# Performance work log

Measured on AMD Instinct MI355X. Metric: run time of the kernel, lower is better.

The kernel has to match this reference:

```python
import jax, jax.numpy as jnp
import numpy as np

B, S, DA, DV, DU, L, M = 16, 256, 1, 32, 1, 4, 12


def conv1x1(x, w, b):
    # x: [B,C,H,W], w: [O,C], b: [O]
    return jnp.einsum('bchw,oc->bohw', x, w) + b[None, :, None, None]


def setup_inputs() -> dict:
    key = jax.random.key(0)
    ks = jax.random.split(key, 12)
    sc = 0.02
    return {
        'x':    jax.random.normal(ks[0], (B, S, S, DA), dtype=jnp.float32),
        'p_w':  sc * jax.random.normal(ks[1], (DV, DA + 2), dtype=jnp.float32),
        'p_b':  sc * jax.random.normal(ks[2], (DV,), dtype=jnp.float32),
        'ws_w': sc * jax.random.normal(ks[3], (L, DV, DV), dtype=jnp.float32),
        'ws_b': sc * jax.random.normal(ks[4], (L, DV), dtype=jnp.float32),
        'w1r':  sc * jax.random.normal(ks[5], (L, DV, DV, M, M), dtype=jnp.float32),
        'w1i':  sc * jax.random.normal(ks[6], (L, DV, DV, M, M), dtype=jnp.float32),
        'w2r':  sc * jax.random.normal(ks[7], (L, DV, DV, M, M), dtype=jnp.float32),
        'w2i':  sc * jax.random.normal(ks[8], (L, DV, DV, M, M), dtype=jnp.float32),
        'q_w':  sc * jax.random.normal(ks[9], (DU, DV), dtype=jnp.float32),
        'q_b':  sc * jax.random.normal(ks[10], (DU,), dtype=jnp.float32),
    }


def fourier_layer(x, w1r, w1i, w2r, w2i):
    # x: [B,C,H,W]; FFT norm None == 'backward' (numpy/jax default)
    b, c, h, w = x.shape
    x_ft = jnp.fft.rfft2(x)                       # [B,C,H,W//2+1] complex
    W1 = w1r + 1j * w1i                           # [C,C,M,M]
    W2 = w2r + 1j * w2i
    top = jnp.einsum('bixy,ioxy->boxy', x_ft[:, :, :M, :M], W1)
    bot = jnp.einsum('bixy,ioxy->boxy', x_ft[:, :, -M:, :M], W2)
    out_ft = jnp.zeros((b, c, h, w // 2 + 1), dtype=x_ft.dtype)
    out_ft = out_ft.at[:, :, :M, :M].set(top)
    out_ft = out_ft.at[:, :, h - M:, :M].set(bot)
    return jnp.fft.irfft2(out_ft, s=(h, w))


def reference(x, p_w, p_b, ws_w, ws_b, w1r, w1i, w2r, w2i, q_w, q_b):
    b, sx, sy, _ = x.shape
    # grid as in get_grid (requires sx == sy, as the original implicitly does)
    gx = jnp.linspace(-1.0, 1.0, sx, dtype=jnp.float32)
    gy = jnp.linspace(-1.0, 1.0, sy, dtype=jnp.float32)
    gridx = jnp.broadcast_to(gx.reshape(1, 1, sx, 1), (b, sy, sx, 1))
    gridy = jnp.broadcast_to(gy.reshape(1, sy, 1, 1), (b, sy, sx, 1))
    grid = jnp.concatenate([gridy, gridx], axis=-1)     # [B,Sy,Sx,2]
    h = jnp.concatenate([x, grid], axis=-1)             # [B,S,S,DA+2]
    h = jnp.transpose(h, (0, 3, 1, 2))                  # NCHW
    h = conv1x1(h, p_w, p_b)                            # lifting
    for i in range(L):
        x1 = fourier_layer(h, w1r[i], w1i[i], w2r[i], w2i[i])
        x2 = conv1x1(h, ws_w[i], ws_b[i])
        h = x1 + x2
        if i < L - 1:
            h = jax.nn.relu(h)
    h = conv1x1(h, q_w, q_b)                            # projection -> [B,1,S,S]
    return jnp.transpose(h, (0, 2, 3, 1)).squeeze(-1)   # [B,S,S]
```

## Files before the change

### kernel.cpp

```cpp
#include <hip/hip_runtime.h>
#include <math.h>

#define NB 16
#define SS 256
#define DV 32
#define MM 12
#define MK 24
#define LL 4
#define TWO_PI_N 0.024543692606170259679f
#define HSTR 257
#define TWSOFF (DV * HSTR)

typedef float v2f __attribute__((ext_vector_type(2)));


__global__ __launch_bounds__(256) void k_prep(const float* __restrict__ ws_w,
        float* __restrict__ twT, float* __restrict__ wT, float* __restrict__ tw2)
{
    int j = threadIdx.x;
    #pragma unroll
    for (int k = 0; k < MM; ++k) {
        float ang = TWO_PI_N * (float)((k * j) & 255);
        float s, c; sincosf(ang, &s, &c);
        twT[j * (MM * 2) + 2 * k]     = c;
        twT[j * (MM * 2) + 2 * k + 1] = -s;
        tw2[(k * SS + j) * 2]     = c;
        tw2[(k * SS + j) * 2 + 1] = s;
    }
    for (int idx = threadIdx.x; idx < LL * DV * DV; idx += 256) {
        int l = idx >> 10, rem = idx & 1023, co = rem >> 5, ci = rem & 31;
        wT[(l * DV + ci) * DV + co] = ws_w[(l * DV + co) * DV + ci];
    }
}

__device__ __forceinline__ void row_dft_from_lds(float* smem,
        const float* __restrict__ twT, float* __restrict__ A,
        int b, int iy, int tid)
{
    int c   = tid & 31;
    int seg = tid >> 5;
    int j0  = seg << 5;

    v2f arai[MM];
    #pragma unroll
    for (int k = 0; k < MM; ++k) arai[k] = (v2f)(0.f);

    const float* hp = smem + c * HSTR + j0;
    #pragma unroll 2
    for (int i = 0; i < 32; ++i) {
        float v = hp[i];
        const v2f* twj = (const v2f*)(twT + (size_t)i * (MM * 2));
        #pragma unroll
        for (int k = 0; k < MM; ++k)
            arai[k] += twj[k] * v;
    }

    const float* ph = smem + TWSOFF + seg * (MM * 2);
    #pragma unroll
    for (int k = 0; k < MM; ++k) {
        float pr = ph[2 * k], pi = ph[2 * k + 1];
        float re = arai[k].x * pr - arai[k].y * pi;
        float im = arai[k].x * pi + arai[k].y * pr;
        arai[k].x = re; arai[k].y = im;
    }

    __syncthreads();
    v2f* red = (v2f*)smem;
    #pragma unroll
    for (int k = 0; k < MM; ++k) red[tid * 13 + k] = arai[k];
    __syncthreads();

    #pragma unroll
    for (int rep = 0; rep < 2; ++rep) {
        int o = tid + rep * 256;
        if (o < 384) {
            int k = o >> 5, cc = o & 31;
            v2f s = (v2f)(0.f);
            #pragma unroll
            for (int sg = 0; sg < 8; ++sg)
                s += red[(sg * 32 + cc) * 13 + k];
            size_t off = ((((size_t)(b * SS + iy)) * MM + k) * DV + cc) * 2;
            A[off]     = s.x;
            A[off + 1] = s.y;
        }
    }
}

__device__ __forceinline__ void build_segphase(float* smem, int tid)
{
    if (tid < 8 * MM) {
        int s = tid / MM, k = tid - s * MM;
        float ang = TWO_PI_N * (float)(((k * s) << 5) & 255);
        float sn, cs; sincosf(ang, &sn, &cs);
        smem[TWSOFF + 2 * tid]     = cs;
        smem[TWSOFF + 2 * tid + 1] = -sn;
    }
}

__global__ __launch_bounds__(256, 4) void k_liftdft(const float* __restrict__ x,
        const float* __restrict__ p_w, const float* __restrict__ p_b,
        float* __restrict__ h, const float* __restrict__ twT, float* __restrict__ A)
{
    __shared__ float smem[DV * HSTR + 8 * MM * 2];
    int tid = threadIdx.x;
    int b  = blockIdx.x >> 8;
    int iy = blockIdx.x & 255;
    int j  = tid;

    build_segphase(smem, tid);

    float xv = x[((size_t)(b * SS + iy)) * SS + j];
    float gy = -1.f + 2.f * (float)iy * (1.f / 255.f);
    float gx = -1.f + 2.f * (float)j  * (1.f / 255.f);

    float* hb = h + ((size_t)b * DV * SS + iy) * SS + j;
    #pragma unroll
    for (int c = 0; c < DV; ++c) {
        float v = p_w[3*c] * xv + p_w[3*c+1] * gy + p_w[3*c+2] * gx + p_b[c];
        *(hb + (size_t)c * SS * SS) = v;
        smem[c * HSTR + j] = v;
    }
    __syncthreads();
    row_dft_from_lds(smem, twT, A, b, iy, tid);
}

__global__ __launch_bounds__(256, 4) void k_ptdft(float* __restrict__ h,
        const float* __restrict__ g, const float* __restrict__ wT,
        const float* __restrict__ ws_b, const float* __restrict__ tw2,
        const float* __restrict__ twT, float* __restrict__ A, int l)
{
    __shared__ float smem[DV * HSTR + 8 * MM * 2];
    int tid = threadIdx.x;
    int b  = blockIdx.x >> 8;
    int iy = blockIdx.x & 255;
    int j  = tid;

    build_segphase(smem, tid);

    float* hb = h + ((size_t)b * DV * SS + iy) * SS + j;
    const float* wt  = wT + (size_t)l * DV * DV;
    const float* wsb = ws_b + (size_t)l * DV;

    float acc[DV];
    #pragma unroll
    for (int co = 0; co < DV; ++co) acc[co] = wsb[co];

    #pragma unroll 4
    for (int ci = 0; ci < DV; ++ci) {
        float hv = *(hb + (size_t)ci * SS * SS);
        const float* wc = wt + ci * DV;
        #pragma unroll
        for (int co = 0; co < DV; ++co) acc[co] += wc[co] * hv;
    }

    const float* gp = g + ((size_t)(b * SS + iy)) * (MM * DV * 2);
    #pragma unroll 2
    for (int ky = 0; ky < MM; ++ky) {
        float2 t2 = *(const float2*)(tw2 + ((size_t)ky * SS + j) * 2);
        const float* Gk = gp + ky * (DV * 2);
        #pragma unroll
        for (int co = 0; co < DV; ++co) {
            float gr = Gk[2 * co], gi = Gk[2 * co + 1];
            acc[co] += gr * t2.x - gi * t2.y;
        }
    }

    #pragma unroll
    for (int co = 0; co < DV; ++co) {
        float v = fmaxf(acc[co], 0.f);
        *(hb + (size_t)co * SS * SS) = v;
        smem[co * HSTR + j] = v;
    }
    __syncthreads();
    row_dft_from_lds(smem, twT, A, b, iy, tid);
}

__global__ __launch_bounds__(256, 4) void k_cm(const float* __restrict__ A,
        const float* __restrict__ w1r, const float* __restrict__ w1i,
        const float* __restrict__ w2r, const float* __restrict__ w2i,
        float* __restrict__ F, int l)
{
    __shared__ float red[4][DV][7][2];
    __shared__ float FinS[DV][6][2];
    int blk = blockIdx.x;
    int mg = blk & 3;
    int bk = blk >> 2;
    int b  = bk / MM;
    int ky = bk - b * MM;
    int tid = threadIdx.x;
    int c = tid & 31, ch = tid >> 5;
    int iy0 = ch * 32;

    const float2* Ap = (const float2*)(A) + ((size_t)(b * SS) * MM + ky) * DV + c;

    float fr[6], fi[6], pc[6], ps[6], sc[6], ssn[6];
    #pragma unroll
    for (int k = 0; k < 6; ++k) {
        int m = mg * 6 + k;
        int f = (m < MM) ? m : (232 + m);
        float s, cc;
        sincosf(TWO_PI_N * (float)f, &s, &cc);
        sc[k] = cc; ssn[k] = s;
        sincosf(TWO_PI_N * (float)((f * iy0) & 255), &s, &cc);
        pc[k] = cc; ps[k] = s;
        fr[k] = fi[k] = 0.f;
    }
    #pragma unroll 4
    for (int i = 0; i < 32; ++i) {
        float2 a = Ap[(size_t)(iy0 + i) * (MM * DV)];
        #pragma unroll
        for (int k = 0; k < 6; ++k) {
            fr[k] += a.x * pc[k] + a.y * ps[k];
            fi[k] += a.y * pc[k] - a.x * ps[k];
            float np = pc[k] * sc[k] - ps[k] * ssn[k];
            float nq = pc[k] * ssn[k] + ps[k] * sc[k];
            pc[k] = np; ps[k] = nq;
        }
    }
    #pragma unroll
    for (int k = 0; k < 6; ++k) {
        fr[k] += __shfl_xor(fr[k], 32, 64);
        fi[k] += __shfl_xor(fi[k], 32, 64);
    }
    int wv = tid >> 6;
    if ((tid & 63) < 32) {
        #pragma unroll
        for (int k = 0; k < 6; ++k) {
            red[wv][c][k][0] = fr[k];
            red[wv][c][k][1] = fi[k];
        }
    }
    __syncthreads();
    if (tid < 192) {
        int cc = tid & 31, k2 = tid >> 5;
        float sr = 0.f, si = 0.f;
        #pragma unroll
        for (int w = 0; w < 4; ++w) {
            sr += red[w][cc][k2][0];
            si += red[w][cc][k2][1];
        }
        FinS[cc][k2][0] = sr; FinS[cc][k2][1] = si;
    }
    __syncthreads();

    int c2 = tid >> 3, ch2 = tid & 7;
    if (ch2 < 6) {
        int o = c2;
        int m = mg * 6 + ch2;
        const float* Wr; const float* Wi; int xm;
        if (m < MM) { Wr = w1r; Wi = w1i; xm = m; }
        else        { Wr = w2r; Wi = w2i; xm = m - MM; }
        float scale = ((ky == 0) ? 1.0f : 2.0f) * (1.0f / 65536.0f);
        float orr = 0.f, oii = 0.f;
        #pragma unroll 4
        for (int i = 0; i < DV; ++i) {
            float gr = FinS[i][ch2][0], gi = FinS[i][ch2][1];
            size_t wi = ((size_t)(l * DV + i) * DV + o) * (MM * MM) + xm * MM + ky;
            float wr = Wr[wi], wim = Wi[wi];
            orr += gr * wr - gi * wim;
            oii += gr * wim + gi * wr;
        }
        size_t off = (((size_t)bk * MK + m) * DV + o) * 2;
        F[off] = orr * scale; F[off + 1] = oii * scale;
    }
}

__global__ __launch_bounds__(384) void k_inv1(const float* __restrict__ F,
        float* __restrict__ g)
{
    __shared__ float itw[MK * 2];
    int tid = threadIdx.x;
    int b = blockIdx.x >> 8, iy = blockIdx.x & 255;
    if (tid < MK) {
        int f = (tid < MM) ? tid : (232 + tid);
        float ang = TWO_PI_N * (float)((f * iy) & 255);
        float s, c; sincosf(ang, &s, &c);
        itw[2 * tid] = c; itw[2 * tid + 1] = s;
    }
    __syncthreads();

    int ky = tid >> 5, co = tid & 31;
    const float* Fp = F + ((size_t)(b * MM + ky) * MK) * (DV * 2) + 2 * co;
    float gr = 0.f, gi = 0.f;
    #pragma unroll
    for (int m = 0; m < MK; ++m) {
        float2 fv = *(const float2*)(Fp + (size_t)m * (DV * 2));
        float ic = itw[2 * m], is = itw[2 * m + 1];
        gr += fv.x * ic - fv.y * is;
        gi += fv.x * is + fv.y * ic;
    }
    size_t o = (((size_t)(b * SS + iy)) * MM + ky) * (DV * 2) + 2 * co;
    g[o] = gr; g[o + 1] = gi;
}

template<int FINAL>
__global__ __launch_bounds__(256, 4) void k_pt(float* __restrict__ h,
        const float* __restrict__ g, const float* __restrict__ wT,
        const float* __restrict__ ws_b, const float* __restrict__ tw2,
        const float* __restrict__ q_w, const float* __restrict__ q_b,
        float* __restrict__ out, int l)
{
    int tid = threadIdx.x;
    int lane = tid & 63;
    int w = __builtin_amdgcn_readfirstlane(tid >> 6);
    int b  = blockIdx.x >> 7;
    int iy = ((blockIdx.x & 127) << 1) + (w >> 1);
    int j0 = ((w & 1) << 7) + (lane << 1);

    float* hb = h + ((size_t)b * DV * SS + iy) * SS + j0;
    const float* wt  = wT + (size_t)l * DV * DV;
    const float* wsb = ws_b + (size_t)l * DV;

    float2 acc[DV];
    #pragma unroll
    for (int co = 0; co < DV; ++co) {
        float bv = wsb[co];
        acc[co].x = bv; acc[co].y = bv;
    }

    #pragma unroll 4
    for (int ci = 0; ci < DV; ++ci) {
        float2 hv = *(const float2*)(hb + (size_t)ci * SS * SS);
        const float* wc = wt + ci * DV;
        #pragma unroll
        for (int co = 0; co < DV; ++co) {
            float wv = wc[co];
            acc[co].x += wv * hv.x; acc[co].y += wv * hv.y;
        }
    }

    const float* gp = g + ((size_t)(b * SS + iy)) * (MM * DV * 2);
    #pragma unroll 2
    for (int ky = 0; ky < MM; ++ky) {
        float4 t4 = *(const float4*)(tw2 + ((size_t)ky * SS + j0) * 2);
        const float* Gk = gp + ky * (DV * 2);
        #pragma unroll
        for (int co = 0; co < DV; ++co) {
            float gr = Gk[2 * co], gi = Gk[2 * co + 1];
            acc[co].x += gr * t4.x - gi * t4.y;
            acc[co].y += gr * t4.z - gi * t4.w;
        }
    }

    if (FINAL) {
        float qb = q_b[0];
        float2 o2; o2.x = qb; o2.y = qb;
        #pragma unroll
        for (int co = 0; co < DV; ++co) {
            float qv = q_w[co];
            o2.x += qv * acc[co].x; o2.y += qv * acc[co].y;
        }
        *(float2*)(out + ((size_t)(b * SS + iy)) * SS + j0) = o2;
    } else {
        #pragma unroll
        for (int co = 0; co < DV; ++co) {
            float2 v;
            v.x = fmaxf(acc[co].x, 0.f); v.y = fmaxf(acc[co].y, 0.f);
            *(float2*)(hb + (size_t)co * SS * SS) = v;
        }
    }
}

extern "C" void kernel_launch(void* const* d_in, const int* in_sizes, int n_in,
                              void* d_out, int out_size, void* d_ws, size_t ws_size,
                              hipStream_t stream)
{
    const float* x    = (const float*)d_in[0];
    const float* p_w  = (const float*)d_in[1];
    const float* p_b  = (const float*)d_in[2];
    const float* ws_w = (const float*)d_in[3];
    const float* ws_b = (const float*)d_in[4];
    const float* w1r  = (const float*)d_in[5];
    const float* w1i  = (const float*)d_in[6];
    const float* w2r  = (const float*)d_in[7];
    const float* w2i  = (const float*)d_in[8];
    const float* q_w  = (const float*)d_in[9];
    const float* q_b  = (const float*)d_in[10];
    float* out = (float*)d_out;

    float* h   = (float*)d_ws;
    float* A   = h   + (size_t)NB * DV * SS * SS;
    float* F   = A   + (size_t)NB * SS * MM * DV * 2;
    float* g   = F   + (size_t)NB * MM * MK * DV * 2;
    float* twT = g   + (size_t)NB * SS * MM * DV * 2;
    float* wT  = twT + (size_t)SS * MM * 2;
    float* tw2 = wT  + (size_t)LL * DV * DV;

    dim3 blk(256);
    k_prep<<<1, blk, 0, stream>>>(ws_w, twT, wT, tw2);
    k_liftdft<<<NB * SS, blk, 0, stream>>>(x, p_w, p_b, h, twT, A);
    for (int l = 0; l < LL; ++l) {
        k_cm<<<NB * MM * 4, blk, 0, stream>>>(A, w1r, w1i, w2r, w2i, F, l);
        k_inv1<<<NB * SS, dim3(384), 0, stream>>>(F, g);
        if (l < LL - 1)
            k_ptdft<<<NB * SS, blk, 0, stream>>>(h, g, wT, ws_b, tw2, twT, A, l);
        else
            k_pt<1><<<NB * 128, blk, 0, stream>>>(h, g, wT, ws_b, tw2,
                                                  q_w, q_b, out, l);
    }
}
```

Before: 677.5 us.

## Fuse inverse column DFT into pointwise kernels via shared memory

Removes the separate k_inv1 launch and the global g buffer. Each pointwise block (k_ptdft and the final projection kernel) now recomputes its row's inverse DFT over the 24 retained modes from F directly into LDS. This drops one launch per layer and the write and read of g, in exchange for extra shared memory, an added barrier and some per-block setup latency.

```diff
diff --git a/kernel.cpp b/kernel.cpp
--- a/kernel.cpp
+++ b/kernel.cpp
@@ -9,7 +9,9 @@
 #define LL 4
 #define TWO_PI_N 0.024543692606170259679f
 #define HSTR 257
-#define TWSOFF (DV * HSTR)
+#define SEGOFF (DV * HSTR)
+#define GOFF   (SEGOFF + 8*MM*2)
+#define ITWOFF (GOFF + MM*DV*2)
 
 typedef float v2f __attribute__((ext_vector_type(2)));
 
@@ -55,7 +57,7 @@
             arai[k] += twj[k] * v;
     }
 
-    const float* ph = smem + TWSOFF + seg * (MM * 2);
+    const float* ph = smem + SEGOFF + seg * (MM * 2);
     #pragma unroll
     for (int k = 0; k < MM; ++k) {
         float pr = ph[2 * k], pi = ph[2 * k + 1];
@@ -92,8 +94,8 @@
         int s = tid / MM, k = tid - s * MM;
         float ang = TWO_PI_N * (float)(((k * s) << 5) & 255);
         float sn, cs; sincosf(ang, &sn, &cs);
-        smem[TWSOFF + 2 * tid]     = cs;
-        smem[TWSOFF + 2 * tid + 1] = -sn;
+        smem[SEGOFF + 2 * tid]     = cs;
+        smem[SEGOFF + 2 * tid + 1] = -sn;
     }
 }
 
@@ -101,7 +103,7 @@
         const float* __restrict__ p_w, const float* __restrict__ p_b,
         float* __restrict__ h, const float* __restrict__ twT, float* __restrict__ A)
 {
-    __shared__ float smem[DV * HSTR + 8 * MM * 2];
+    __shared__ float smem[SEGOFF + 8 * MM * 2];
     int tid = threadIdx.x;
     int b  = blockIdx.x >> 8;
     int iy = blockIdx.x & 255;
@@ -125,17 +127,43 @@
 }
 
 __global__ __launch_bounds__(256, 4) void k_ptdft(float* __restrict__ h,
-        const float* __restrict__ g, const float* __restrict__ wT,
+        const float* __restrict__ F, const float* __restrict__ wT,
         const float* __restrict__ ws_b, const float* __restrict__ tw2,
         const float* __restrict__ twT, float* __restrict__ A, int l)
 {
-    __shared__ float smem[DV * HSTR + 8 * MM * 2];
+    __shared__ float smem[ITWOFF + MK * 2];
     int tid = threadIdx.x;
     int b  = blockIdx.x >> 8;
     int iy = blockIdx.x & 255;
     int j  = tid;
 
     build_segphase(smem, tid);
+    if (tid < MK) {
+        int f = (tid < MM) ? tid : (232 + tid);
+        float s, c; sincosf(TWO_PI_N * (float)((f * iy) & 255), &s, &c);
+        smem[ITWOFF + 2 * tid]     = c;
+        smem[ITWOFF + 2 * tid + 1] = s;
+    }
+    __syncthreads();
+
+    #pragma unroll
+    for (int rep = 0; rep < 2; ++rep) {
+        int o = tid + rep * 256;
+        if (o < MM * DV) {
+            int ky = o >> 5, co = o & 31;
+            const float* Fp = F + ((size_t)(b * MM + ky) * MK) * (DV * 2) + 2 * co;
+            float gr = 0.f, gi = 0.f;
+            #pragma unroll
+            for (int m = 0; m < MK; ++m) {
+                float2 fv = *(const float2*)(Fp + (size_t)m * (DV * 2));
+                float ic = smem[ITWOFF + 2 * m], is = smem[ITWOFF + 2 * m + 1];
+                gr += fv.x * ic - fv.y * is;
+                gi += fv.x * is + fv.y * ic;
+            }
+            smem[GOFF + 2 * o]     = gr;
+            smem[GOFF + 2 * o + 1] = gi;
+        }
+    }
 
     float* hb = h + ((size_t)b * DV * SS + iy) * SS + j;
     const float* wt  = wT + (size_t)l * DV * DV;
@@ -153,11 +181,12 @@
         for (int co = 0; co < DV; ++co) acc[co] += wc[co] * hv;
     }
 
-    const float* gp = g + ((size_t)(b * SS + iy)) * (MM * DV * 2);
+    __syncthreads();
+
     #pragma unroll 2
     for (int ky = 0; ky < MM; ++ky) {
         float2 t2 = *(const float2*)(tw2 + ((size_t)ky * SS + j) * 2);
-        const float* Gk = gp + ky * (DV * 2);
+        const float* Gk = smem + GOFF + ky * (DV * 2);
         #pragma unroll
         for (int co = 0; co < DV; ++co) {
             float gr = Gk[2 * co], gi = Gk[2 * co + 1];
@@ -265,47 +294,47 @@
     }
 }
 
-__global__ __launch_bounds__(384) void k_inv1(const float* __restrict__ F,
-        float* __restrict__ g)
-{
-    __shared__ float itw[MK * 2];
-    int tid = threadIdx.x;
-    int b = blockIdx.x >> 8, iy = blockIdx.x & 255;
-    if (tid < MK) {
-        int f = (tid < MM) ? tid : (232 + tid);
-        float ang = TWO_PI_N * (float)((f * iy) & 255);
-        float s, c; sincosf(ang, &s, &c);
-        itw[2 * tid] = c; itw[2 * tid + 1] = s;
-    }
-    __syncthreads();
-
-    int ky = tid >> 5, co = tid & 31;
-    const float* Fp = F + ((size_t)(b * MM + ky) * MK) * (DV * 2) + 2 * co;
-    float gr = 0.f, gi = 0.f;
-    #pragma unroll
-    for (int m = 0; m < MK; ++m) {
-        float2 fv = *(const float2*)(Fp + (size_t)m * (DV * 2));
-        float ic = itw[2 * m], is = itw[2 * m + 1];
-        gr += fv.x * ic - fv.y * is;
-        gi += fv.x * is + fv.y * ic;
-    }
-    size_t o = (((size_t)(b * SS + iy)) * MM + ky) * (DV * 2) + 2 * co;
-    g[o] = gr; g[o + 1] = gi;
-}
-
-template<int FINAL>
-__global__ __launch_bounds__(256, 4) void k_pt(float* __restrict__ h,
-        const float* __restrict__ g, const float* __restrict__ wT,
+__global__ __launch_bounds__(256, 4) void k_ptfin(float* __restrict__ h,
+        const float* __restrict__ F, const float* __restrict__ wT,
         const float* __restrict__ ws_b, const float* __restrict__ tw2,
         const float* __restrict__ q_w, const float* __restrict__ q_b,
         float* __restrict__ out, int l)
 {
+    __shared__ float s2[2 * MK * 2 + 2 * MM * DV * 2];
     int tid = threadIdx.x;
     int lane = tid & 63;
     int w = __builtin_amdgcn_readfirstlane(tid >> 6);
-    int b  = blockIdx.x >> 7;
-    int iy = ((blockIdx.x & 127) << 1) + (w >> 1);
-    int j0 = ((w & 1) << 7) + (lane << 1);
+    int b   = blockIdx.x >> 7;
+    int iyb = (blockIdx.x & 127) << 1;
+    int iy  = iyb + (w >> 1);
+    int j0  = ((w & 1) << 7) + (lane << 1);
+
+    if (tid < 2 * MK) {
+        int r = tid / MK, m = tid - r * MK;
+        int f = (m < MM) ? m : (232 + m);
+        float s, c; sincosf(TWO_PI_N * (float)((f * (iyb + r)) & 255), &s, &c);
+        s2[2 * tid] = c; s2[2 * tid + 1] = s;
+    }
+    __syncthreads();
+
+    #pragma unroll
+    for (int rep = 0; rep < 3; ++rep) {
+        int o = rep * 256 + tid;
+        int r = o / 384, oo = o - r * 384;
+        int ky = oo >> 5, co = oo & 31;
+        const float* Fp = F + ((size_t)(b * MM + ky) * MK) * (DV * 2) + 2 * co;
+        const float* itw = s2 + r * (MK * 2);
+        float gr = 0.f, gi = 0.f;
+        #pragma unroll
+        for (int m = 0; m < MK; ++m) {
+            float2 fv = *(const float2*)(Fp + (size_t)m * (DV * 2));
+            float ic = itw[2 * m], is = itw[2 * m + 1];
+            gr += fv.x * ic - fv.y * is;
+            gi += fv.x * is + fv.y * ic;
+        }
+        s2[2 * MK * 2 + 2 * o]     = gr;
+        s2[2 * MK * 2 + 2 * o + 1] = gi;
+    }
 
     float* hb = h + ((size_t)b * DV * SS + iy) * SS + j0;
     const float* wt  = wT + (size_t)l * DV * DV;
@@ -329,7 +358,9 @@
         }
     }
 
-    const float* gp = g + ((size_t)(b * SS + iy)) * (MM * DV * 2);
+    __syncthreads();
+
+    const float* gp = s2 + 2 * MK * 2 + (size_t)(w >> 1) * (MM * DV * 2);
     #pragma unroll 2
     for (int ky = 0; ky < MM; ++ky) {
         float4 t4 = *(const float4*)(tw2 + ((size_t)ky * SS + j0) * 2);
@@ -342,23 +373,14 @@
         }
     }
 
-    if (FINAL) {
-        float qb = q_b[0];
-        float2 o2; o2.x = qb; o2.y = qb;
-        #pragma unroll
-        for (int co = 0; co < DV; ++co) {
-            float qv = q_w[co];
-            o2.x += qv * acc[co].x; o2.y += qv * acc[co].y;
-        }
-        *(float2*)(out + ((size_t)(b * SS + iy)) * SS + j0) = o2;
-    } else {
-        #pragma unroll
-        for (int co = 0; co < DV; ++co) {
-            float2 v;
-            v.x = fmaxf(acc[co].x, 0.f); v.y = fmaxf(acc[co].y, 0.f);
-            *(float2*)(hb + (size_t)co * SS * SS) = v;
-        }
-    }
+    float qb = q_b[0];
+    float2 o2; o2.x = qb; o2.y = qb;
+    #pragma unroll
+    for (int co = 0; co < DV; ++co) {
+        float qv = q_w[co];
+        o2.x += qv * acc[co].x; o2.y += qv * acc[co].y;
+    }
+    *(float2*)(out + ((size_t)(b * SS + iy)) * SS + j0) = o2;
 }
 
 extern "C" void kernel_launch(void* const* d_in, const int* in_sizes, int n_in,
@@ -381,8 +403,7 @@
     float* h   = (float*)d_ws;
     float* A   = h   + (size_t)NB * DV * SS * SS;
     float* F   = A   + (size_t)NB * SS * MM * DV * 2;
-    float* g   = F   + (size_t)NB * MM * MK * DV * 2;
-    float* twT = g   + (size_t)NB * SS * MM * DV * 2;
+    float* twT = F   + (size_t)NB * MM * MK * DV * 2;
     float* wT  = twT + (size_t)SS * MM * 2;
     float* tw2 = wT  + (size_t)LL * DV * DV;
 
@@ -391,11 +412,10 @@
     k_liftdft<<<NB * SS, blk, 0, stream>>>(x, p_w, p_b, h, twT, A);
     for (int l = 0; l < LL; ++l) {
         k_cm<<<NB * MM * 4, blk, 0, stream>>>(A, w1r, w1i, w2r, w2i, F, l);
-        k_inv1<<<NB * SS, dim3(384), 0, stream>>>(F, g);
         if (l < LL - 1)
-            k_ptdft<<<NB * SS, blk, 0, stream>>>(h, g, wT, ws_b, tw2, twT, A, l);
+            k_ptdft<<<NB * SS, blk, 0, stream>>>(h, F, wT, ws_b, tw2, twT, A, l);
         else
-            k_pt<1><<<NB * 128, blk, 0, stream>>>(h, g, wT, ws_b, tw2,
+            k_ptfin<<<NB * 128, blk, 0, stream>>>(h, F, wT, ws_b, tw2,
                                                   q_w, q_b, out, l);
     }
 }
```

Result: slower. 719.8 us (+6.2%).

## Fuse column DFT, mode mixing and inverse column DFT into one kernel

Applied to the files above, without the earlier changes.

Merges k_cm and k_inv1 into a single kernel k_cmg, with one block per (batch, ky) computing all 24 modes instead of splitting them across 4 blocks. The mixed spectrum is kept in LDS and each thread then evaluates the inverse column transform for one row. This removes the F intermediate buffer round-trip and one launch per layer. The trade-off is a grid that shrinks from 768 to 192 blocks, with more registers per thread (24 twiddle accumulators and 32 complex outputs), so there is less parallelism across the GPU.

```diff
diff --git a/kernel.cpp b/kernel.cpp
--- a/kernel.cpp
+++ b/kernel.cpp
@@ -9,7 +9,7 @@
 #define LL 4
 #define TWO_PI_N 0.024543692606170259679f
 #define HSTR 257
-#define TWSOFF (DV * HSTR)
+#define SEGOFF (DV * HSTR)
 
 typedef float v2f __attribute__((ext_vector_type(2)));
 
@@ -55,7 +55,7 @@
             arai[k] += twj[k] * v;
     }
 
-    const float* ph = smem + TWSOFF + seg * (MM * 2);
+    const float* ph = smem + SEGOFF + seg * (MM * 2);
     #pragma unroll
     for (int k = 0; k < MM; ++k) {
         float pr = ph[2 * k], pi = ph[2 * k + 1];
@@ -92,8 +92,8 @@
         int s = tid / MM, k = tid - s * MM;
         float ang = TWO_PI_N * (float)(((k * s) << 5) & 255);
         float sn, cs; sincosf(ang, &sn, &cs);
-        smem[TWSOFF + 2 * tid]     = cs;
-        smem[TWSOFF + 2 * tid + 1] = -sn;
+        smem[SEGOFF + 2 * tid]     = cs;
+        smem[SEGOFF + 2 * tid + 1] = -sn;
     }
 }
 
@@ -101,7 +101,7 @@
         const float* __restrict__ p_w, const float* __restrict__ p_b,
         float* __restrict__ h, const float* __restrict__ twT, float* __restrict__ A)
 {
-    __shared__ float smem[DV * HSTR + 8 * MM * 2];
+    __shared__ float smem[SEGOFF + 8 * MM * 2];
     int tid = threadIdx.x;
     int b  = blockIdx.x >> 8;
     int iy = blockIdx.x & 255;
@@ -129,7 +129,7 @@
         const float* __restrict__ ws_b, const float* __restrict__ tw2,
         const float* __restrict__ twT, float* __restrict__ A, int l)
 {
-    __shared__ float smem[DV * HSTR + 8 * MM * 2];
+    __shared__ float smem[SEGOFF + 8 * MM * 2];
     int tid = threadIdx.x;
     int b  = blockIdx.x >> 8;
     int iy = blockIdx.x & 255;
@@ -175,16 +175,15 @@
     row_dft_from_lds(smem, twT, A, b, iy, tid);
 }
 
-__global__ __launch_bounds__(256, 4) void k_cm(const float* __restrict__ A,
+__global__ __launch_bounds__(256) void k_cmg(const float* __restrict__ A,
         const float* __restrict__ w1r, const float* __restrict__ w1i,
         const float* __restrict__ w2r, const float* __restrict__ w2i,
-        float* __restrict__ F, int l)
-{
-    __shared__ float red[4][DV][7][2];
-    __shared__ float FinS[DV][6][2];
-    int blk = blockIdx.x;
-    int mg = blk & 3;
-    int bk = blk >> 2;
+        float* __restrict__ g, int l)
+{
+    __shared__ float red[4][DV][25][2];
+    __shared__ float FinS[DV][25][2];
+    __shared__ float FLDS[MK][DV][2];
+    int bk = blockIdx.x;
     int b  = bk / MM;
     int ky = bk - b * MM;
     int tid = threadIdx.x;
@@ -193,11 +192,10 @@
 
     const float2* Ap = (const float2*)(A) + ((size_t)(b * SS) * MM + ky) * DV + c;
 
-    float fr[6], fi[6], pc[6], ps[6], sc[6], ssn[6];
-    #pragma unroll
-    for (int k = 0; k < 6; ++k) {
-        int m = mg * 6 + k;
-        int f = (m < MM) ? m : (232 + m);
+    float fr[MK], fi[MK], pc[MK], ps[MK], sc[MK], ssn[MK];
+    #pragma unroll
+    for (int k = 0; k < MK; ++k) {
+        int f = (k < MM) ? k : (232 + k);
         float s, cc;
         sincosf(TWO_PI_N * (float)f, &s, &cc);
         sc[k] = cc; ssn[k] = s;
@@ -205,11 +203,11 @@
         pc[k] = cc; ps[k] = s;
         fr[k] = fi[k] = 0.f;
     }
-    #pragma unroll 4
+    #pragma unroll 2
     for (int i = 0; i < 32; ++i) {
         float2 a = Ap[(size_t)(iy0 + i) * (MM * DV)];
         #pragma unroll
-        for (int k = 0; k < 6; ++k) {
+        for (int k = 0; k < MK; ++k) {
             fr[k] += a.x * pc[k] + a.y * ps[k];
             fi[k] += a.y * pc[k] - a.x * ps[k];
             float np = pc[k] * sc[k] - ps[k] * ssn[k];
@@ -218,21 +216,23 @@
         }
     }
     #pragma unroll
-    for (int k = 0; k < 6; ++k) {
+    for (int k = 0; k < MK; ++k) {
         fr[k] += __shfl_xor(fr[k], 32, 64);
         fi[k] += __shfl_xor(fi[k], 32, 64);
     }
     int wv = tid >> 6;
     if ((tid & 63) < 32) {
         #pragma unroll
-        for (int k = 0; k < 6; ++k) {
+        for (int k = 0; k < MK; ++k) {
             red[wv][c][k][0] = fr[k];
             red[wv][c][k][1] = fi[k];
         }
     }
     __syncthreads();
-    if (tid < 192) {
-        int cc = tid & 31, k2 = tid >> 5;
+    #pragma unroll
+    for (int rep = 0; rep < 3; ++rep) {
+        int idx = rep * 256 + tid;
+        int cc = idx & 31, k2 = idx >> 5;
         float sr = 0.f, si = 0.f;
         #pragma unroll
         for (int w = 0; w < 4; ++w) {
@@ -243,54 +243,52 @@
     }
     __syncthreads();
 
-    int c2 = tid >> 3, ch2 = tid & 7;
-    if (ch2 < 6) {
-        int o = c2;
-        int m = mg * 6 + ch2;
+    float scale = ((ky == 0) ? 1.0f : 2.0f) * (1.0f / 65536.0f);
+    #pragma unroll
+    for (int rep = 0; rep < 3; ++rep) {
+        int idx = rep * 256 + tid;
+        int o = idx & 31, m = idx >> 5;
         const float* Wr; const float* Wi; int xm;
         if (m < MM) { Wr = w1r; Wi = w1i; xm = m; }
         else        { Wr = w2r; Wi = w2i; xm = m - MM; }
-        float scale = ((ky == 0) ? 1.0f : 2.0f) * (1.0f / 65536.0f);
         float orr = 0.f, oii = 0.f;
         #pragma unroll 4
         for (int i = 0; i < DV; ++i) {
-            float gr = FinS[i][ch2][0], gi = FinS[i][ch2][1];
+            float gr = FinS[i][m][0], gi = FinS[i][m][1];
             size_t wi = ((size_t)(l * DV + i) * DV + o) * (MM * MM) + xm * MM + ky;
             float wr = Wr[wi], wim = Wi[wi];
             orr += gr * wr - gi * wim;
             oii += gr * wim + gi * wr;
         }
-        size_t off = (((size_t)bk * MK + m) * DV + o) * 2;
-        F[off] = orr * scale; F[off + 1] = oii * scale;
-    }
-}
-
-__global__ __launch_bounds__(384) void k_inv1(const float* __restrict__ F,
-        float* __restrict__ g)
-{
-    __shared__ float itw[MK * 2];
-    int tid = threadIdx.x;
-    int b = blockIdx.x >> 8, iy = blockIdx.x & 255;
-    if (tid < MK) {
-        int f = (tid < MM) ? tid : (232 + tid);
-        float ang = TWO_PI_N * (float)((f * iy) & 255);
-        float s, c; sincosf(ang, &s, &c);
-        itw[2 * tid] = c; itw[2 * tid + 1] = s;
-    }
-    __syncthreads();
-
-    int ky = tid >> 5, co = tid & 31;
-    const float* Fp = F + ((size_t)(b * MM + ky) * MK) * (DV * 2) + 2 * co;
-    float gr = 0.f, gi = 0.f;
+        FLDS[m][o][0] = orr * scale;
+        FLDS[m][o][1] = oii * scale;
+    }
+    __syncthreads();
+
+    int iy = tid;
+    float twc[MK], tws[MK];
     #pragma unroll
     for (int m = 0; m < MK; ++m) {
-        float2 fv = *(const float2*)(Fp + (size_t)m * (DV * 2));
-        float ic = itw[2 * m], is = itw[2 * m + 1];
-        gr += fv.x * ic - fv.y * is;
-        gi += fv.x * is + fv.y * ic;
-    }
-    size_t o = (((size_t)(b * SS + iy)) * MM + ky) * (DV * 2) + 2 * co;
-    g[o] = gr; g[o + 1] = gi;
+        int f = (m < MM) ? m : (232 + m);
+        float s, cc; sincosf(TWO_PI_N * (float)((f * iy) & 255), &s, &cc);
+        twc[m] = cc; tws[m] = s;
+    }
+    float2 gacc[DV];
+    #pragma unroll
+    for (int co = 0; co < DV; ++co) { gacc[co].x = 0.f; gacc[co].y = 0.f; }
+    for (int m = 0; m < MK; ++m) {
+        float ic = twc[m], is = tws[m];
+        #pragma unroll
+        for (int co = 0; co < DV; ++co) {
+            float2 fv = *(const float2*)&FLDS[m][co][0];
+            gacc[co].x += fv.x * ic - fv.y * is;
+            gacc[co].y += fv.x * is + fv.y * ic;
+        }
+    }
+    float* go = g + (((size_t)(b * SS + iy)) * MM + ky) * (DV * 2);
+    #pragma unroll
+    for (int co = 0; co < DV; ++co)
+        *(float2*)(go + 2 * co) = gacc[co];
 }
 
 template<int FINAL>
@@ -380,8 +378,7 @@
 
     float* h   = (float*)d_ws;
     float* A   = h   + (size_t)NB * DV * SS * SS;
-    float* F   = A   + (size_t)NB * SS * MM * DV * 2;
-    float* g   = F   + (size_t)NB * MM * MK * DV * 2;
+    float* g   = A   + (size_t)NB * SS * MM * DV * 2;
     float* twT = g   + (size_t)NB * SS * MM * DV * 2;
     float* wT  = twT + (size_t)SS * MM * 2;
     float* tw2 = wT  + (size_t)LL * DV * DV;
@@ -390,8 +387,7 @@
     k_prep<<<1, blk, 0, stream>>>(ws_w, twT, wT, tw2);
     k_liftdft<<<NB * SS, blk, 0, stream>>>(x, p_w, p_b, h, twT, A);
     for (int l = 0; l < LL; ++l) {
-        k_cm<<<NB * MM * 4, blk, 0, stream>>>(A, w1r, w1i, w2r, w2i, F, l);
-        k_inv1<<<NB * SS, dim3(384), 0, stream>>>(F, g);
+        k_cmg<<<NB * MM, blk, 0, stream>>>(A, w1r, w1i, w2r, w2i, g, l);
         if (l < LL - 1)
             k_ptdft<<<NB * SS, blk, 0, stream>>>(h, g, wT, ws_b, tw2, twT, A, l);
         else
```

Result: slower. 739.0 us (+9.1%).

## Split row DFT into two 16-channel halves with shuffle-based reduction

Applied to the files above, without the earlier changes.

The row-DFT epilogue now stages only 16 channels at a time in LDS, which roughly halves the shared memory footprint and could allow more resident blocks. Each thread covers 16 columns instead of 32, and partial sums are reduced with wavefront xor-shuffles before a small LDS cross-wave reduction. The cost is an extra pass with more barriers, while channel values have to stay live in registers across both halves.

```diff
diff --git a/kernel.cpp b/kernel.cpp
--- a/kernel.cpp
+++ b/kernel.cpp
@@ -9,7 +9,10 @@
 #define LL 4
 #define TWO_PI_N 0.024543692606170259679f
 #define HSTR 257
-#define TWSOFF (DV * HSTR)
+#define H16   (16 * HSTR)
+#define SEGO  H16
+#define REDO  (H16 + 16 * MM * 2)
+#define LDSF  (REDO + 4 * 16 * 13 * 2)
 
 typedef float v2f __attribute__((ext_vector_type(2)));
 
@@ -33,67 +36,78 @@
     }
 }
 
-__device__ __forceinline__ void row_dft_from_lds(float* smem,
+__device__ __forceinline__ void build_segphase16(float* smem, int tid)
+{
+    if (tid < 16 * MM) {
+        int s = tid / MM, k = tid - s * MM;
+        float ang = TWO_PI_N * (float)(((k * s) << 4) & 255);
+        float sn, cs; sincosf(ang, &sn, &cs);
+        smem[SEGO + 2 * tid]     = cs;
+        smem[SEGO + 2 * tid + 1] = -sn;
+    }
+}
+
+__device__ __forceinline__ void row_dft_epilogue(float* smem,
         const float* __restrict__ twT, float* __restrict__ A,
-        int b, int iy, int tid)
-{
-    int c   = tid & 31;
-    int seg = tid >> 5;
-    int j0  = seg << 5;
-
-    v2f arai[MM];
-    #pragma unroll
-    for (int k = 0; k < MM; ++k) arai[k] = (v2f)(0.f);
-
-    const float* hp = smem + c * HSTR + j0;
-    #pragma unroll 2
-    for (int i = 0; i < 32; ++i) {
-        float v = hp[i];
-        const v2f* twj = (const v2f*)(twT + (size_t)i * (MM * 2));
-        #pragma unroll
-        for (int k = 0; k < MM; ++k)
-            arai[k] += twj[k] * v;
-    }
-
-    const float* ph = smem + TWSOFF + seg * (MM * 2);
-    #pragma unroll
-    for (int k = 0; k < MM; ++k) {
-        float pr = ph[2 * k], pi = ph[2 * k + 1];
-        float re = arai[k].x * pr - arai[k].y * pi;
-        float im = arai[k].x * pi + arai[k].y * pr;
-        arai[k].x = re; arai[k].y = im;
-    }
-
-    __syncthreads();
-    v2f* red = (v2f*)smem;
-    #pragma unroll
-    for (int k = 0; k < MM; ++k) red[tid * 13 + k] = arai[k];
-    __syncthreads();
-
-    #pragma unroll
-    for (int rep = 0; rep < 2; ++rep) {
-        int o = tid + rep * 256;
-        if (o < 384) {
-            int k = o >> 5, cc = o & 31;
+        const float* acc, int b, int iy, int tid)
+{
+    int cc  = tid & 15;
+    int seg = tid >> 4;
+    int j   = tid;
+    size_t abase = ((size_t)(b * SS + iy)) * MM;
+    v2f* red = (v2f*)(smem + REDO);
+    int w = tid >> 6;
+
+    #pragma unroll
+    for (int half = 0; half < 2; ++half) {
+        #pragma unroll
+        for (int c = 0; c < 16; ++c)
+            smem[c * HSTR + j] = acc[half * 16 + c];
+        __syncthreads();
+
+        v2f arai[MM];
+        #pragma unroll
+        for (int k = 0; k < MM; ++k) arai[k] = (v2f)(0.f);
+        const float* hp = smem + cc * HSTR + seg * 16;
+        #pragma unroll 2
+        for (int i = 0; i < 16; ++i) {
+            float v = hp[i];
+            const v2f* twj = (const v2f*)(twT + (size_t)i * (MM * 2));
+            #pragma unroll
+            for (int k = 0; k < MM; ++k)
+                arai[k] += twj[k] * v;
+        }
+        const float* ph = smem + SEGO + seg * (MM * 2);
+        #pragma unroll
+        for (int k = 0; k < MM; ++k) {
+            float pr = ph[2 * k], pi = ph[2 * k + 1];
+            float re = arai[k].x * pr - arai[k].y * pi;
+            float im = arai[k].x * pi + arai[k].y * pr;
+            arai[k].x = re; arai[k].y = im;
+        }
+        #pragma unroll
+        for (int k = 0; k < MM; ++k) {
+            arai[k].x += __shfl_xor(arai[k].x, 16, 64);
+            arai[k].y += __shfl_xor(arai[k].y, 16, 64);
+            arai[k].x += __shfl_xor(arai[k].x, 32, 64);
+            arai[k].y += __shfl_xor(arai[k].y, 32, 64);
+        }
+        if ((tid & 48) == 0) {
+            #pragma unroll
+            for (int k = 0; k < MM; ++k)
+                red[(w * 16 + cc) * 13 + k] = arai[k];
+        }
+        __syncthreads();
+        if (tid < 192) {
+            int k2 = tid >> 4, c2 = tid & 15;
             v2f s = (v2f)(0.f);
             #pragma unroll
-            for (int sg = 0; sg < 8; ++sg)
-                s += red[(sg * 32 + cc) * 13 + k];
-            size_t off = ((((size_t)(b * SS + iy)) * MM + k) * DV + cc) * 2;
+            for (int wv = 0; wv < 4; ++wv)
+                s += red[(wv * 16 + c2) * 13 + k2];
+            size_t off = ((abase + k2) * DV + half * 16 + c2) * 2;
             A[off]     = s.x;
             A[off + 1] = s.y;
         }
-    }
-}
-
-__device__ __forceinline__ void build_segphase(float* smem, int tid)
-{
-    if (tid < 8 * MM) {
-        int s = tid / MM, k = tid - s * MM;
-        float ang = TWO_PI_N * (float)(((k * s) << 5) & 255);
-        float sn, cs; sincosf(ang, &sn, &cs);
-        smem[TWSOFF + 2 * tid]     = cs;
-        smem[TWSOFF + 2 * tid + 1] = -sn;
     }
 }
 
@@ -101,27 +115,26 @@
         const float* __restrict__ p_w, const float* __restrict__ p_b,
         float* __restrict__ h, const float* __restrict__ twT, float* __restrict__ A)
 {
-    __shared__ float smem[DV * HSTR + 8 * MM * 2];
+    __shared__ float smem[LDSF];
     int tid = threadIdx.x;
     int b  = blockIdx.x >> 8;
     int iy = blockIdx.x & 255;
     int j  = tid;
 
-    build_segphase(smem, tid);
+    build_segphase16(smem, tid);
 
     float xv = x[((size_t)(b * SS + iy)) * SS + j];
     float gy = -1.f + 2.f * (float)iy * (1.f / 255.f);
     float gx = -1.f + 2.f * (float)j  * (1.f / 255.f);
 
     float* hb = h + ((size_t)b * DV * SS + iy) * SS + j;
+    float hv[DV];
     #pragma unroll
     for (int c = 0; c < DV; ++c) {
-        float v = p_w[3*c] * xv + p_w[3*c+1] * gy + p_w[3*c+2] * gx + p_b[c];
-        *(hb + (size_t)c * SS * SS) = v;
-        smem[c * HSTR + j] = v;
-    }
-    __syncthreads();
-    row_dft_from_lds(smem, twT, A, b, iy, tid);
+        hv[c] = p_w[3*c] * xv + p_w[3*c+1] * gy + p_w[3*c+2] * gx + p_b[c];
+        *(hb + (size_t)c * SS * SS) = hv[c];
+    }
+    row_dft_epilogue(smem, twT, A, hv, b, iy, tid);
 }
 
 __global__ __launch_bounds__(256, 4) void k_ptdft(float* __restrict__ h,
@@ -129,13 +142,13 @@
         const float* __restrict__ ws_b, const float* __restrict__ tw2,
         const float* __restrict__ twT, float* __restrict__ A, int l)
 {
-    __shared__ float smem[DV * HSTR + 8 * MM * 2];
+    __shared__ float smem[LDSF];
     int tid = threadIdx.x;
     int b  = blockIdx.x >> 8;
     int iy = blockIdx.x & 255;
     int j  = tid;
 
-    build_segphase(smem, tid);
+    build_segphase16(smem, tid);
 
     float* hb = h + ((size_t)b * DV * SS + iy) * SS + j;
     const float* wt  = wT + (size_t)l * DV * DV;
@@ -167,12 +180,10 @@
 
     #pragma unroll
     for (int co = 0; co < DV; ++co) {
-        float v = fmaxf(acc[co], 0.f);
-        *(hb + (size_t)co * SS * SS) = v;
-        smem[co * HSTR + j] = v;
-    }
-    __syncthreads();
-    row_dft_from_lds(smem, twT, A, b, iy, tid);
+        acc[co] = fmaxf(acc[co], 0.f);
+        *(hb + (size_t)co * SS * SS) = acc[co];
+    }
+    row_dft_epilogue(smem, twT, A, acc, b, iy, tid);
 }
 
 __global__ __launch_bounds__(256, 4) void k_cm(const float* __restrict__ A,
```

Result: slower. 715.3 us (+5.6%).
